# Optimization experiments

Hardware: AMD Instinct MI355X
Metric: run time of the kernel (lower is better)

The kernel has to match this reference:

```python
import jax, jax.numpy as jnp
import numpy as np

LEAKY_SLOPE = 0.2  # PyG GATv2Conv default negative_slope


def gatv2_layer(x, src, dst, Wl, Wr, att, bias, concat):
    """PyG GATv2Conv (eval mode, dropout off, self-loops already in src/dst).
    x: [N, Din]; Wl/Wr: [Din, H*C]; att: [H, C]; bias: [H*C] or [C].
    """
    N = x.shape[0]
    H, C = att.shape
    xl = (x @ Wl).reshape(N, H, C)   # source transform
    xr = (x @ Wr).reshape(N, H, C)   # target transform
    # per-edge GATv2 score: att . leakyrelu(x_l[j] + x_r[i])
    e = jax.nn.leaky_relu(xl[src] + xr[dst], negative_slope=LEAKY_SLOPE)  # [E, H, C]
    score = jnp.einsum('ehc,hc->eh', e, att)                              # [E, H]
    # segment softmax over incoming edges of each dst node
    m = jax.ops.segment_max(score, dst, num_segments=N)                   # [N, H]
    a = jnp.exp(score - m[dst])
    denom = jax.ops.segment_sum(a, dst, num_segments=N)                   # [N, H]
    alpha = a / denom[dst]                                                # [E, H]
    out = jax.ops.segment_sum(xl[src] * alpha[..., None], dst, num_segments=N)  # [N, H, C]
    out = out.reshape(N, H * C) if concat else out.mean(axis=1)
    return out + bias


def setup_inputs() -> dict:
    key = jax.random.key(0)
    ks = jax.random.split(key, 10)
    N, D, E = 20000, 128, 320000
    HID, HEADS, OUT = 64, 8, 32
    x = jax.random.normal(ks[0], (N, D), dtype=jnp.float32)
    edge_index = jax.random.randint(ks[1], (2, E), 0, N)
    glorot = lambda k, shape, fan: jax.random.normal(k, shape, jnp.float32) * (1.0 / np.sqrt(fan))
    W1l = glorot(ks[2], (D, HEADS * HID), D)
    W1r = glorot(ks[3], (D, HEADS * HID), D)
    att1 = glorot(ks[4], (HEADS, HID), HID)
    b1 = jnp.zeros((HEADS * HID,), jnp.float32)
    W2l = glorot(ks[5], (HEADS * HID, 64), HEADS * HID)
    W2r = glorot(ks[6], (HEADS * HID, 64), HEADS * HID)
    att2 = glorot(ks[7], (1, 64), 64)
    b2 = jnp.zeros((64,), jnp.float32)
    Wlin = glorot(ks[8], (64, OUT), 64)
    blin = jnp.zeros((OUT,), jnp.float32)
    return {"x": x, "edge_index": edge_index, "W1l": W1l, "W1r": W1r, "att1": att1,
            "b1": b1, "W2l": W2l, "W2r": W2r, "att2": att2, "b2": b2,
            "Wlin": Wlin, "blin": blin}


def reference(x, edge_index, W1l, W1r, att1, b1, W2l, W2r, att2, b2, Wlin, blin):
    N = x.shape[0]
    loop = jnp.arange(N)
    src = jnp.concatenate([edge_index[0], loop])  # PyG add_self_loops=True
    dst = jnp.concatenate([edge_index[1], loop])
    h = jax.nn.elu(gatv2_layer(x, src, dst, W1l, W1r, att1, b1, concat=True))
    h = jax.nn.elu(gatv2_layer(h, src, dst, W2l, W2r, att2, b2, concat=False))
    return jax.nn.elu(h @ Wlin + blin)
```

## Files before the change

kernel.cpp:

```cpp
#include <hip/hip_runtime.h>
#include <hip/hip_bf16.h>

typedef __attribute__((ext_vector_type(8))) short short8;
typedef __attribute__((ext_vector_type(4))) short short4v;
typedef __attribute__((ext_vector_type(4))) float floatx4;
typedef __attribute__((ext_vector_type(2))) float float2v;
typedef __attribute__((ext_vector_type(4))) int int4v;
typedef __attribute__((ext_vector_type(2))) int int2v;

#define LOG2E 1.44269504f

__device__ __forceinline__ float b2f(short s) {
    unsigned u = ((unsigned)(unsigned short)s) << 16;
    float f; __builtin_memcpy(&f, &u, 4); return f;
}
__device__ __forceinline__ short f2b(float f) {
    __hip_bfloat16 hb = __float2bfloat16(f);
    unsigned short us; __builtin_memcpy(&us, &hb, 2);
    return (short)us;
}
__device__ __forceinline__ float2v bpair(int p) {
    unsigned ulo = ((unsigned)p) << 16;
    unsigned uhi = ((unsigned)p) & 0xFFFF0000u;
    float flo, fhi;
    __builtin_memcpy(&flo, &ulo, 4);
    __builtin_memcpy(&fhi, &uhi, 4);
    float2v r; r.x = flo; r.y = fhi; return r;
}

__device__ __forceinline__ float2v pk_add(float2v a, float2v b) {
    float2v d;
    asm("v_pk_add_f32 %0, %1, %2" : "=v"(d) : "v"(a), "v"(b));
    return d;
}
__device__ __forceinline__ float2v pk_fma(float2v a, float2v b, float2v c) {
    float2v d;
    asm("v_pk_fma_f32 %0, %1, %2, %3" : "=v"(d) : "v"(a), "v"(b), "v"(c));
    return d;
}
__device__ __forceinline__ float2v pk_abs(float2v a) {
    float2v d;
    d.x = __builtin_fabsf(a.x);
    d.y = __builtin_fabsf(a.y);
    return d;
}

template<int CTRL>
__device__ __forceinline__ float dppadd(float x) {
    int xi; __builtin_memcpy(&xi, &x, 4);
    int yi = __builtin_amdgcn_update_dpp(0, xi, CTRL, 0xF, 0xF, false);
    float y; __builtin_memcpy(&y, &yi, 4);
    return x + y;
}
__device__ __forceinline__ float red8(float x) {
    x = dppadd<0xB1>(x);
    x = dppadd<0x4E>(x);
    x = dppadd<0x141>(x);
    return x;
}
__device__ __forceinline__ float red16(float x) {
    return dppadd<0x140>(red8(x));
}

__global__ void prep_all(const float* __restrict__ x,
                         const float* __restrict__ W1l, const float* __restrict__ W1r,
                         const float* __restrict__ W2l, const float* __restrict__ W2r,
                         short* __restrict__ xb, short* __restrict__ w1t,
                         short* __restrict__ w2t, int nx4,
                         const int* __restrict__ esrc, const int* __restrict__ edst,
                         int E, int N, int* __restrict__ counts, int* __restrict__ srcs) {
    int tid = blockIdx.x * blockDim.x + threadIdx.x;
    int ET = E + N;
    if (tid < ET) {
        int d, s;
        if (tid < E) { d = edst[tid]; s = esrc[tid]; }
        else { d = tid - E; s = d; }
        int pos = atomicAdd(&counts[d], 1);
        if (pos < 64) srcs[(d << 6) + pos] = s;
    }
    int idx = tid;
    if (idx < nx4) {
        floatx4 v = *(const floatx4*)(x + idx * 4);
        short4v o; o[0] = f2b(v[0]); o[1] = f2b(v[1]); o[2] = f2b(v[2]); o[3] = f2b(v[3]);
        *(short4v*)(xb + idx * 4) = o;
        return;
    }
    idx -= nx4;
    if (idx < 131072) {
        int n = idx >> 7, k = idx & 127;
        float v = (n < 512) ? W1l[k * 512 + n] : W1r[k * 512 + (n - 512)];
        w1t[idx] = f2b(v);
        return;
    }
    idx -= 131072;
    if (idx < 65536) {
        int n = idx >> 9, k = idx & 511;
        float v = (n < 64) ? W2l[k * 64 + n] : W2r[k * 64 + (n - 64)];
        w2t[idx] = f2b(v);
    }
}

__global__ __launch_bounds__(256) void gemm1(const short* __restrict__ A,
                                             const short* __restrict__ Bt,
                                             short* __restrict__ xl1, short* __restrict__ xr1,
                                             int M) {
    __shared__ short As[64 * 136];
    __shared__ short Bs[128 * 136];
    int t = threadIdx.x;
    int w = t >> 6, L = t & 63, q = L >> 4, s = L & 15;
    int p = blockIdx.x + (blockIdx.y << 3);
    int my = gridDim.y;
    int ww = (p & 7) * my + (p >> 3);
    int M0 = (ww >> 3) * 64, N0 = (ww & 7) * 128;
    #pragma unroll
    for (int i = 0; i < 4; ++i) {
        int c = t + i * 256;
        int r = c >> 4, col = (c & 15) * 8;
        int gr = M0 + r;
        short8 v = {};
        if (gr < M) v = *(const short8*)(A + (size_t)gr * 128 + col);
        *(short8*)(&As[r * 136 + col]) = v;
    }
    #pragma unroll
    for (int i = 0; i < 8; ++i) {
        int c = t + i * 256;
        int r = c >> 4, col = (c & 15) * 8;
        short8 v = *(const short8*)(Bt + (size_t)(N0 + r) * 128 + col);
        *(short8*)(&Bs[r * 136 + col]) = v;
    }
    __syncthreads();
    short8 a[4];
    #pragma unroll
    for (int kk = 0; kk < 4; ++kk)
        a[kk] = *(const short8*)(&As[(w * 16 + s) * 136 + kk * 32 + q * 8]);
    floatx4 acc[8] = {};
    #pragma unroll
    for (int tt = 0; tt < 8; ++tt) {
        #pragma unroll
        for (int kk = 0; kk < 4; ++kk) {
            short8 b = *(const short8*)(&Bs[(tt * 16 + s) * 136 + kk * 32 + q * 8]);
            acc[tt] = __builtin_amdgcn_mfma_f32_16x16x32_bf16(a[kk], b, acc[tt], 0, 0, 0);
        }
    }
    __syncthreads();
    #pragma unroll
    for (int tt = 0; tt < 8; ++tt) {
        #pragma unroll
        for (int rg = 0; rg < 4; ++rg) {
            int rl = w * 16 + q * 4 + rg;
            As[rl * 136 + tt * 16 + s] = f2b(acc[tt][rg]);
        }
    }
    __syncthreads();
    short* Cb = (N0 < 512) ? xl1 : xr1;
    int cb = (N0 < 512) ? N0 : N0 - 512;
    #pragma unroll
    for (int i = 0; i < 4; ++i) {
        int c = t + i * 256;
        int r = c >> 4, col = (c & 15) * 8;
        int row = M0 + r;
        if (row < M) {
            short8 v = *(const short8*)(&As[r * 136 + col]);
            *(short8*)(Cb + (size_t)row * 512 + cb + col) = v;
        }
    }
}

__global__ __launch_bounds__(256) void gemm2(const short* __restrict__ A,
                                             const short* __restrict__ Bt,
                                             short* __restrict__ C, int M) {
    __shared__ short As[32 * 72];
    __shared__ short Bs[64 * 72];
    int t = threadIdx.x;
    int w = t >> 6, L = t & 63, q = L >> 4, s = L & 15;
    int rw = (w >> 1) * 16, cw = (w & 1) * 32;
    int p = blockIdx.x + gridDim.x * blockIdx.y;
    int nwg = gridDim.x * 2;
    int qq = nwg >> 3, rr = nwg & 7;
    int kx = p & 7, tx = p >> 3;
    int ww = (kx < rr ? kx * (qq + 1) : rr * (qq + 1) + (kx - rr) * qq) + tx;
    int M0 = (ww >> 1) * 32, N0 = (ww & 1) * 64;
    floatx4 acc[2] = {};
    for (int k0 = 0; k0 < 512; k0 += 64) {
        {
            int r = t >> 3, col = (t & 7) * 8;
            int gr = M0 + r;
            short8 v = {};
            if (gr < M) v = *(const short8*)(A + (size_t)gr * 512 + k0 + col);
            *(short8*)(&As[r * 72 + col]) = v;
        }
        #pragma unroll
        for (int i = 0; i < 2; ++i) {
            int c = t + i * 256;
            int r = c >> 3, col = (c & 7) * 8;
            short8 v = *(const short8*)(Bt + (size_t)(N0 + r) * 512 + k0 + col);
            *(short8*)(&Bs[r * 72 + col]) = v;
        }
        __syncthreads();
        #pragma unroll
        for (int kk = 0; kk < 2; ++kk) {
            short8 a = *(const short8*)(&As[(rw + s) * 72 + kk * 32 + q * 8]);
            #pragma unroll
            for (int tt = 0; tt < 2; ++tt) {
                short8 b = *(const short8*)(&Bs[(cw + tt * 16 + s) * 72 + kk * 32 + q * 8]);
                acc[tt] = __builtin_amdgcn_mfma_f32_16x16x32_bf16(a, b, acc[tt], 0, 0, 0);
            }
        }
        __syncthreads();
    }
    #pragma unroll
    for (int tt = 0; tt < 2; ++tt) {
        #pragma unroll
        for (int rg = 0; rg < 4; ++rg) {
            int rl = rw + q * 4 + rg;
            As[rl * 72 + cw + tt * 16 + s] = f2b(acc[tt][rg]);
        }
    }
    __syncthreads();
    {
        int r = t >> 3, col = (t & 7) * 8;
        int row = M0 + r;
        if (row < M) {
            short8 v = *(const short8*)(&As[r * 72 + col]);
            *(short8*)(C + (size_t)row * 128 + N0 + col) = v;
        }
    }
}

__global__ __launch_bounds__(256) void gat_l1(const short* __restrict__ xl,
                       const short* __restrict__ xr,
                       const int* __restrict__ counts, const int* __restrict__ srcs,
                       const float* __restrict__ att, const float* __restrict__ bias,
                       short* __restrict__ h1, int Nn) {
    int i = (blockIdx.x * blockDim.x + threadIdx.x) >> 6;
    if (i >= Nn) return;
    int L = threadIdx.x & 63;
    int c0 = L * 8;
    float2v xrv[4], at6[4], at4[4];
    {
        float av[8];
        *(floatx4*)av       = *(const floatx4*)(att + c0);
        *(floatx4*)(av + 4) = *(const floatx4*)(att + c0 + 4);
        int4v x4 = *(const int4v*)(xr + (i << 9) + c0);
        #pragma unroll
        for (int c = 0; c < 4; ++c) {
            xrv[c] = bpair(x4[c]);
            at6[c].x = av[2 * c]     * (0.6f * LOG2E);
            at6[c].y = av[2 * c + 1] * (0.6f * LOG2E);
            at4[c].x = av[2 * c]     * (0.4f * LOG2E);
            at4[c].y = av[2 * c + 1] * (0.4f * LOG2E);
        }
    }
    const int4v* xl4 = (const int4v*)xl;
    int jv = srcs[(i << 6) + L];
    int deg = counts[i]; deg = deg > 64 ? 64 : deg;
    float2v acc[4] = {};
    float dnm = 0.f;

    auto ldrow = [&](int e) -> int4v {
        int ee = e < deg ? e : 0;
        unsigned j = (unsigned)__builtin_amdgcn_readlane(jv, ee);
        return xl4[((size_t)j << 6) + L];
    };
    auto edge = [&](int4v a4, bool valid) {
        float2v v[4]; float2v pp = {};
        #pragma unroll
        for (int c = 0; c < 4; ++c) {
            v[c] = bpair(a4[c]);
            float2v t = pk_add(v[c], xrv[c]);
            pp = pk_fma(at6[c], t, pp);
            pp = pk_fma(at4[c], pk_abs(t), pp);
        }
        float e2 = __builtin_amdgcn_exp2f(red8(pp.x + pp.y));
        e2 = valid ? e2 : 0.f;
        dnm += e2;
        float2v ev; ev.x = e2; ev.y = e2;
        #pragma unroll
        for (int c = 0; c < 4; ++c)
            acc[c] = pk_fma(ev, v[c], acc[c]);
    };

    int4v b0 = ldrow(0), b1 = ldrow(1);
    int e = 0;
    for (; e + 3 < deg; e += 2) {
        int4v n0 = ldrow(e + 2), n1 = ldrow(e + 3);
        edge(b0, true);
        edge(b1, true);
        b0 = n0; b1 = n1;
    }
    {
        int4v b2 = ldrow(e + 2);
        edge(b0, true);
        edge(b1, e + 1 < deg);
        edge(b2, e + 2 < deg);
    }

    float inv = 1.f / dnm;
    float bv[8];
    *(floatx4*)bv       = *(const floatx4*)(bias + c0);
    *(floatx4*)(bv + 4) = *(const floatx4*)(bias + c0 + 4);
    short8 o8;
    #pragma unroll
    for (int c = 0; c < 4; ++c) {
        float ox = fmaf(acc[c].x, inv, bv[2 * c]);
        float oy = fmaf(acc[c].y, inv, bv[2 * c + 1]);
        ox = ox > 0.f ? ox : __expf(ox) - 1.f;
        oy = oy > 0.f ? oy : __expf(oy) - 1.f;
        o8[2 * c] = f2b(ox);
        o8[2 * c + 1] = f2b(oy);
    }
    *(short8*)(h1 + (i << 9) + c0) = o8;
}

__global__ __launch_bounds__(256) void gat_l2_fin(const short* __restrict__ x2,
                        const int* __restrict__ counts, const int* __restrict__ srcs,
                        const float* __restrict__ att, const float* __restrict__ bias,
                        const float* __restrict__ Wlin, const float* __restrict__ blin,
                        float* __restrict__ out, int Nn) {
    __shared__ float Ws[2048];
    __shared__ float bs[32];
    __shared__ float h2s[4][64];
    int t = threadIdx.x;
    for (int idx = t; idx < 2048; idx += 256) Ws[idx] = Wlin[idx];
    if (t < 32) bs[t] = blin[t];
    __syncthreads();
    int w = t >> 6, L = t & 63;
    int i = blockIdx.x * 4 + w;
    if (i >= Nn) return;
    int g = L >> 4;
    int lc = L & 15;
    int c4 = lc * 4;
    float2v xrv[2], at6[2], at4[2];
    {
        int2v xv = *(const int2v*)(x2 + (i << 7) + 64 + c4);
        xrv[0] = bpair(xv.x);
        xrv[1] = bpair(xv.y);
        floatx4 a4 = *(const floatx4*)(att + c4);
        at6[0].x = a4[0] * (0.6f * LOG2E); at6[0].y = a4[1] * (0.6f * LOG2E);
        at6[1].x = a4[2] * (0.6f * LOG2E); at6[1].y = a4[3] * (0.6f * LOG2E);
        at4[0].x = a4[0] * (0.4f * LOG2E); at4[0].y = a4[1] * (0.4f * LOG2E);
        at4[1].x = a4[2] * (0.4f * LOG2E); at4[1].y = a4[3] * (0.4f * LOG2E);
    }
    float dnm = 0.f;
    float2v acc0 = {}, acc1 = {};
    int kb = i << 6;
    int deg = counts[i]; deg = deg > 64 ? 64 : deg;
    int ke = kb + deg;
    const int2v* x2i = (const int2v*)x2;

    auto doedge = [&](int2v Vv, bool val) {
        float2v v0 = bpair(Vv.x), v1 = bpair(Vv.y);
        float2v t0 = pk_add(v0, xrv[0]), t1 = pk_add(v1, xrv[1]);
        float2v pp = pk_fma(at6[0], t0, at4[0] * pk_abs(t0));
        pp = pk_fma(at6[1], t1, pp);
        pp = pk_fma(at4[1], pk_abs(t1), pp);
        float e = val ? __builtin_amdgcn_exp2f(red16(pp.x + pp.y)) : 0.f;
        dnm += e;
        float2v e2; e2.x = e; e2.y = e;
        acc0 = pk_fma(e2, v0, acc0);
        acc1 = pk_fma(e2, v1, acc1);
    };

    for (int k0 = kb; k0 < ke; k0 += 16) {
        int ka = k0 + g, kc = k0 + 4 + g, kd = k0 + 8 + g, kf = k0 + 12 + g;
        bool va = ka < ke, vb = kc < ke, vc = kd < ke, vd = kf < ke;
        int ja = srcs[va ? ka : kb];
        int jb = srcs[vb ? kc : kb];
        int jc = srcs[vc ? kd : kb];
        int jd = srcs[vd ? kf : kb];
        int2v Va = x2i[(ja << 5) + lc];
        int2v Vb = x2i[(jb << 5) + lc];
        int2v Vc = x2i[(jc << 5) + lc];
        int2v Vd = x2i[(jd << 5) + lc];
        doedge(Va, va);
        doedge(Vb, vb);
        doedge(Vc, vc);
        doedge(Vd, vd);
    }
    #pragma unroll
    for (int m = 16; m <= 32; m <<= 1) {
        dnm += __shfl_xor(dnm, m, 64);
        acc0.x += __shfl_xor(acc0.x, m, 64);
        acc0.y += __shfl_xor(acc0.y, m, 64);
        acc1.x += __shfl_xor(acc1.x, m, 64);
        acc1.y += __shfl_xor(acc1.y, m, 64);
    }
    float inv = 1.f / dnm;
    floatx4 bv = *(const floatx4*)(bias + c4);
    float o0 = fmaf(acc0.x, inv, bv[0]);
    float o1 = fmaf(acc0.y, inv, bv[1]);
    float o2 = fmaf(acc1.x, inv, bv[2]);
    float o3 = fmaf(acc1.y, inv, bv[3]);
    o0 = o0 > 0.f ? o0 : __expf(o0) - 1.f;
    o1 = o1 > 0.f ? o1 : __expf(o1) - 1.f;
    o2 = o2 > 0.f ? o2 : __expf(o2) - 1.f;
    o3 = o3 > 0.f ? o3 : __expf(o3) - 1.f;
    if (L < 16) {
        floatx4 hv; hv[0] = o0; hv[1] = o1; hv[2] = o2; hv[3] = o3;
        *(floatx4*)(&h2s[w][c4]) = hv;
    }
    int oc = L & 31;
    float accl = 0.f;
    #pragma unroll
    for (int kk = 0; kk < 16; ++kk) {
        floatx4 h = *(const floatx4*)(&h2s[w][kk * 4]);
        accl = fmaf(h[0], Ws[(kk * 4 + 0) * 32 + oc], accl);
        accl = fmaf(h[1], Ws[(kk * 4 + 1) * 32 + oc], accl);
        accl = fmaf(h[2], Ws[(kk * 4 + 2) * 32 + oc], accl);
        accl = fmaf(h[3], Ws[(kk * 4 + 3) * 32 + oc], accl);
    }
    if (L < 32) {
        float r = accl + bs[oc];
        r = r > 0.f ? r : __expf(r) - 1.f;
        out[(size_t)i * 32 + oc] = r;
    }
}

extern "C" void kernel_launch(void* const* d_in, const int* in_sizes, int n_in,
                              void* d_out, int out_size, void* d_ws, size_t ws_size,
                              hipStream_t stream) {
    const float* x    = (const float*)d_in[0];
    const int*   ei   = (const int*)d_in[1];
    const float* W1l  = (const float*)d_in[2];
    const float* W1r  = (const float*)d_in[3];
    const float* att1 = (const float*)d_in[4];
    const float* b1   = (const float*)d_in[5];
    const float* W2l  = (const float*)d_in[6];
    const float* W2r  = (const float*)d_in[7];
    const float* att2 = (const float*)d_in[8];
    const float* b2   = (const float*)d_in[9];
    const float* Wlin = (const float*)d_in[10];
    const float* blin = (const float*)d_in[11];

    const int N  = in_sizes[0] / 128;
    const int E  = in_sizes[1] / 2;

    char* w = (char*)d_ws;
    size_t cur = 0;
    auto take = [&](size_t bytes) -> void* {
        void* p = w + cur;
        cur = (cur + bytes + 255) & ~(size_t)255;
        return p;
    };
    int*   counts = (int*)take((size_t)N * 4);
    int*   srcs   = (int*)take((size_t)N * 64 * 4);
    short* xb     = (short*)take((size_t)N * 128 * 2);
    short* w1t    = (short*)take((size_t)1024 * 128 * 2);
    short* w2t    = (short*)take((size_t)128 * 512 * 2);
    short* xl1    = (short*)take((size_t)N * 512 * 2);
    short* xr1    = (short*)take((size_t)N * 512 * 2);
    short* h1     = (short*)take((size_t)N * 512 * 2);
    short* x2     = (short*)take((size_t)N * 128 * 2);

    hipMemsetAsync(counts, 0, (size_t)N * 4, stream);
    int nx4 = N * 32;
    int nconv = nx4 + 131072 + 65536;
    int nprep = (E + N) > nconv ? (E + N) : nconv;
    prep_all<<<(nprep + 255) / 256, 256, 0, stream>>>(x, W1l, W1r, W2l, W2r, xb, w1t, w2t,
                                                      nx4, ei, ei + E, E, N, counts, srcs);

    gemm1<<<dim3(8, (N + 63) / 64), 256, 0, stream>>>(xb, w1t, xl1, xr1, N);
    gat_l1<<<(N + 3) / 4, 256, 0, stream>>>(xl1, xr1, counts, srcs, att1, b1, h1, N);

    gemm2<<<dim3((N + 31) / 32, 2), 256, 0, stream>>>(h1, w2t, x2, N);
    gat_l2_fin<<<(N + 3) / 4, 256, 0, stream>>>(x2, counts, srcs, att2, b2, Wlin, blin,
                                                (float*)d_out, N);
}
```

Measured before the change: 200.8 us.

## Use head-major layout for layer-1 features and split GAT layer 1 per head

Layer-1 xl/xr/h1 buffers are stored head-major ([H][N][64]) so each gat_l1 block handles one head for four nodes. Each wave processes 8 edges in parallel with 8 lanes per edge and reduces across the edge groups with shuffles, instead of one wave walking edges serially over the full 512-wide row. Source indices are stored as 16-bit values to halve adjacency traffic. The per-head split is meant to improve cache locality of the gathers, since each head slice is smaller, and to expose more parallelism, at the cost of eight times more blocks and extra shuffle reductions. The 16-bit indices rely on N fitting in 65536.

```diff
diff --git a/kernel.cpp b/kernel.cpp
--- a/kernel.cpp
+++ b/kernel.cpp
@@ -10,10 +10,6 @@
 
 #define LOG2E 1.44269504f
 
-__device__ __forceinline__ float b2f(short s) {
-    unsigned u = ((unsigned)(unsigned short)s) << 16;
-    float f; __builtin_memcpy(&f, &u, 4); return f;
-}
 __device__ __forceinline__ short f2b(float f) {
     __hip_bfloat16 hb = __float2bfloat16(f);
     unsigned short us; __builtin_memcpy(&us, &hb, 2);
@@ -68,7 +64,8 @@
                          short* __restrict__ xb, short* __restrict__ w1t,
                          short* __restrict__ w2t, int nx4,
                          const int* __restrict__ esrc, const int* __restrict__ edst,
-                         int E, int N, int* __restrict__ counts, int* __restrict__ srcs) {
+                         int E, int N, int* __restrict__ counts,
+                         unsigned short* __restrict__ srcs) {
     int tid = blockIdx.x * blockDim.x + threadIdx.x;
     int ET = E + N;
     if (tid < ET) {
@@ -76,7 +73,7 @@
         if (tid < E) { d = edst[tid]; s = esrc[tid]; }
         else { d = tid - E; s = d; }
         int pos = atomicAdd(&counts[d], 1);
-        if (pos < 64) srcs[(d << 6) + pos] = s;
+        if (pos < 64) srcs[(d << 6) + pos] = (unsigned short)s;
     }
     int idx = tid;
     if (idx < nx4) {
@@ -154,6 +151,7 @@
     __syncthreads();
     short* Cb = (N0 < 512) ? xl1 : xr1;
     int cb = (N0 < 512) ? N0 : N0 - 512;
+    size_t M64 = (size_t)M * 64;
     #pragma unroll
     for (int i = 0; i < 4; ++i) {
         int c = t + i * 256;
@@ -161,7 +159,8 @@
         int row = M0 + r;
         if (row < M) {
             short8 v = *(const short8*)(&As[r * 136 + col]);
-            *(short8*)(Cb + (size_t)row * 512 + cb + col) = v;
+            int cc = cb + col;
+            *(short8*)(Cb + (size_t)(cc >> 6) * M64 + (size_t)row * 64 + (cc & 63)) = v;
         }
     }
 }
@@ -180,13 +179,14 @@
     int kx = p & 7, tx = p >> 3;
     int ww = (kx < rr ? kx * (qq + 1) : rr * (qq + 1) + (kx - rr) * qq) + tx;
     int M0 = (ww >> 1) * 32, N0 = (ww & 1) * 64;
+    size_t M64 = (size_t)M * 64;
     floatx4 acc[2] = {};
     for (int k0 = 0; k0 < 512; k0 += 64) {
         {
             int r = t >> 3, col = (t & 7) * 8;
             int gr = M0 + r;
             short8 v = {};
-            if (gr < M) v = *(const short8*)(A + (size_t)gr * 512 + k0 + col);
+            if (gr < M) v = *(const short8*)(A + (size_t)(k0 >> 6) * M64 + (size_t)gr * 64 + col);
             *(short8*)(&As[r * 72 + col]) = v;
         }
         #pragma unroll
@@ -227,21 +227,28 @@
     }
 }
 
-__global__ __launch_bounds__(256) void gat_l1(const short* __restrict__ xl,
-                       const short* __restrict__ xr,
-                       const int* __restrict__ counts, const int* __restrict__ srcs,
+__global__ __launch_bounds__(256) void gat_l1(const short* __restrict__ xlh,
+                       const short* __restrict__ xrh,
+                       const int* __restrict__ counts,
+                       const unsigned short* __restrict__ srcs,
                        const float* __restrict__ att, const float* __restrict__ bias,
-                       short* __restrict__ h1, int Nn) {
-    int i = (blockIdx.x * blockDim.x + threadIdx.x) >> 6;
+                       short* __restrict__ h1h, int Nn) {
+    int bid = blockIdx.x;
+    int h = bid & 7, nb = bid >> 3;
+    int t = threadIdx.x;
+    int w = t >> 6, L = t & 63;
+    int i = nb * 4 + w;
     if (i >= Nn) return;
-    int L = threadIdx.x & 63;
-    int c0 = L * 8;
+    int g = L >> 3;
+    int o8 = (L & 7) * 8;
+    size_t slice = (size_t)h * ((size_t)Nn * 64);
+    const short* Bh = xlh + slice;
     float2v xrv[4], at6[4], at4[4];
     {
         float av[8];
-        *(floatx4*)av       = *(const floatx4*)(att + c0);
-        *(floatx4*)(av + 4) = *(const floatx4*)(att + c0 + 4);
-        int4v x4 = *(const int4v*)(xr + (i << 9) + c0);
+        *(floatx4*)av       = *(const floatx4*)(att + h * 64 + o8);
+        *(floatx4*)(av + 4) = *(const floatx4*)(att + h * 64 + o8 + 4);
+        int4v x4 = *(const int4v*)(xrh + slice + (size_t)i * 64 + o8);
         #pragma unroll
         for (int c = 0; c < 4; ++c) {
             xrv[c] = bpair(x4[c]);
@@ -251,28 +258,30 @@
             at4[c].y = av[2 * c + 1] * (0.4f * LOG2E);
         }
     }
-    const int4v* xl4 = (const int4v*)xl;
     int jv = srcs[(i << 6) + L];
     int deg = counts[i]; deg = deg > 64 ? 64 : deg;
     float2v acc[4] = {};
     float dnm = 0.f;
 
-    auto ldrow = [&](int e) -> int4v {
-        int ee = e < deg ? e : 0;
-        unsigned j = (unsigned)__builtin_amdgcn_readlane(jv, ee);
-        return xl4[((size_t)j << 6) + L];
+    auto fetchj = [&](int e) -> int {
+        int idx = e + g;
+        idx = idx < deg ? idx : 0;
+        return __shfl(jv, idx, 64);
     };
-    auto edge = [&](int4v a4, bool valid) {
+    auto ldrow = [&](int j) -> int4v {
+        return *(const int4v*)(Bh + (((unsigned)j) << 6) + o8);
+    };
+    auto process = [&](int4v a4, int e) {
         float2v v[4]; float2v pp = {};
         #pragma unroll
         for (int c = 0; c < 4; ++c) {
             v[c] = bpair(a4[c]);
-            float2v t = pk_add(v[c], xrv[c]);
-            pp = pk_fma(at6[c], t, pp);
-            pp = pk_fma(at4[c], pk_abs(t), pp);
+            float2v tv = pk_add(v[c], xrv[c]);
+            pp = pk_fma(at6[c], tv, pp);
+            pp = pk_fma(at4[c], pk_abs(tv), pp);
         }
         float e2 = __builtin_amdgcn_exp2f(red8(pp.x + pp.y));
-        e2 = valid ? e2 : 0.f;
+        e2 = (e + g < deg) ? e2 : 0.f;
         dnm += e2;
         float2v ev; ev.x = e2; ev.y = e2;
         #pragma unroll
@@ -280,40 +289,49 @@
             acc[c] = pk_fma(ev, v[c], acc[c]);
     };
 
-    int4v b0 = ldrow(0), b1 = ldrow(1);
+    int4v cur = ldrow(fetchj(0));
     int e = 0;
-    for (; e + 3 < deg; e += 2) {
-        int4v n0 = ldrow(e + 2), n1 = ldrow(e + 3);
-        edge(b0, true);
-        edge(b1, true);
-        b0 = n0; b1 = n1;
-    }
-    {
-        int4v b2 = ldrow(e + 2);
-        edge(b0, true);
-        edge(b1, e + 1 < deg);
-        edge(b2, e + 2 < deg);
-    }
-
-    float inv = 1.f / dnm;
-    float bv[8];
-    *(floatx4*)bv       = *(const floatx4*)(bias + c0);
-    *(floatx4*)(bv + 4) = *(const floatx4*)(bias + c0 + 4);
-    short8 o8;
+    for (; e + 8 < deg; e += 8) {
+        int4v nxt = ldrow(fetchj(e + 8));
+        process(cur, e);
+        cur = nxt;
+    }
+    process(cur, e);
+
+    dnm += __shfl_xor(dnm, 8, 64);
+    dnm += __shfl_xor(dnm, 16, 64);
+    dnm += __shfl_xor(dnm, 32, 64);
     #pragma unroll
     for (int c = 0; c < 4; ++c) {
-        float ox = fmaf(acc[c].x, inv, bv[2 * c]);
-        float oy = fmaf(acc[c].y, inv, bv[2 * c + 1]);
-        ox = ox > 0.f ? ox : __expf(ox) - 1.f;
-        oy = oy > 0.f ? oy : __expf(oy) - 1.f;
-        o8[2 * c] = f2b(ox);
-        o8[2 * c + 1] = f2b(oy);
-    }
-    *(short8*)(h1 + (i << 9) + c0) = o8;
+        acc[c].x += __shfl_xor(acc[c].x, 8, 64);
+        acc[c].x += __shfl_xor(acc[c].x, 16, 64);
+        acc[c].x += __shfl_xor(acc[c].x, 32, 64);
+        acc[c].y += __shfl_xor(acc[c].y, 8, 64);
+        acc[c].y += __shfl_xor(acc[c].y, 16, 64);
+        acc[c].y += __shfl_xor(acc[c].y, 32, 64);
+    }
+    if (g == 0) {
+        float inv = 1.f / dnm;
+        float bv[8];
+        *(floatx4*)bv       = *(const floatx4*)(bias + h * 64 + o8);
+        *(floatx4*)(bv + 4) = *(const floatx4*)(bias + h * 64 + o8 + 4);
+        short8 ov;
+        #pragma unroll
+        for (int c = 0; c < 4; ++c) {
+            float ox = fmaf(acc[c].x, inv, bv[2 * c]);
+            float oy = fmaf(acc[c].y, inv, bv[2 * c + 1]);
+            ox = ox > 0.f ? ox : __expf(ox) - 1.f;
+            oy = oy > 0.f ? oy : __expf(oy) - 1.f;
+            ov[2 * c] = f2b(ox);
+            ov[2 * c + 1] = f2b(oy);
+        }
+        *(short8*)(h1h + slice + (size_t)i * 64 + o8) = ov;
+    }
 }
 
 __global__ __launch_bounds__(256) void gat_l2_fin(const short* __restrict__ x2,
-                        const int* __restrict__ counts, const int* __restrict__ srcs,
+                        const int* __restrict__ counts,
+                        const unsigned short* __restrict__ srcs,
                         const float* __restrict__ att, const float* __restrict__ bias,
                         const float* __restrict__ Wlin, const float* __restrict__ blin,
                         float* __restrict__ out, int Nn) {
@@ -403,11 +421,11 @@
     float accl = 0.f;
     #pragma unroll
     for (int kk = 0; kk < 16; ++kk) {
-        floatx4 h = *(const floatx4*)(&h2s[w][kk * 4]);
-        accl = fmaf(h[0], Ws[(kk * 4 + 0) * 32 + oc], accl);
-        accl = fmaf(h[1], Ws[(kk * 4 + 1) * 32 + oc], accl);
-        accl = fmaf(h[2], Ws[(kk * 4 + 2) * 32 + oc], accl);
-        accl = fmaf(h[3], Ws[(kk * 4 + 3) * 32 + oc], accl);
+        floatx4 hvv = *(const floatx4*)(&h2s[w][kk * 4]);
+        accl = fmaf(hvv[0], Ws[(kk * 4 + 0) * 32 + oc], accl);
+        accl = fmaf(hvv[1], Ws[(kk * 4 + 1) * 32 + oc], accl);
+        accl = fmaf(hvv[2], Ws[(kk * 4 + 2) * 32 + oc], accl);
+        accl = fmaf(hvv[3], Ws[(kk * 4 + 3) * 32 + oc], accl);
     }
     if (L < 32) {
         float r = accl + bs[oc];
@@ -442,8 +460,8 @@
         cur = (cur + bytes + 255) & ~(size_t)255;
         return p;
     };
-    int*   counts = (int*)take((size_t)N * 4);
-    int*   srcs   = (int*)take((size_t)N * 64 * 4);
+    int*            counts = (int*)take((size_t)N * 4);
+    unsigned short* srcs   = (unsigned short*)take((size_t)N * 64 * 2);
     short* xb     = (short*)take((size_t)N * 128 * 2);
     short* w1t    = (short*)take((size_t)1024 * 128 * 2);
     short* w2t    = (short*)take((size_t)128 * 512 * 2);
@@ -460,7 +478,7 @@
                                                       nx4, ei, ei + E, E, N, counts, srcs);
 
     gemm1<<<dim3(8, (N + 63) / 64), 256, 0, stream>>>(xb, w1t, xl1, xr1, N);
-    gat_l1<<<(N + 3) / 4, 256, 0, stream>>>(xl1, xr1, counts, srcs, att1, b1, h1, N);
+    gat_l1<<<8 * ((N + 3) / 4), 256, 0, stream>>>(xl1, xr1, counts, srcs, att1, b1, h1, N);
 
     gemm2<<<dim3((N + 31) / 32, 2), 256, 0, stream>>>(h1, w2t, x2, N);
     gat_l2_fin<<<(N + 3) / 4, 256, 0, stream>>>(x2, counts, srcs, att2, b2, Wlin, blin,
```

New measurement: 217.2 us. 8.2% more time.
